# Optimization experiments

Measured on AMD Instinct MI355X. Metric: run time of the kernel, lower is better.

## Reference

```python
import jax, jax.numpy as jnp
import numpy as np

N_NODES = 100000
N_EDGES = 1600000
N_PAIRS = 1000000
IN_CH = 32
HID = 32


def glorot(key, shape):
    lim = float(np.sqrt(6.0 / (shape[0] + shape[1])))
    return jax.random.uniform(key, shape, jnp.float32, -lim, lim)


def setup_inputs() -> dict:
    key = jax.random.key(0)
    ks = jax.random.split(key, 9)
    x = jax.random.normal(ks[0], (N_NODES, IN_CH), jnp.float32)
    edge_index = jax.random.randint(ks[1], (2, N_EDGES), 0, N_NODES, jnp.int64)
    edge_pairs = jax.random.randint(ks[2], (N_PAIRS, 2), 0, N_NODES, jnp.int64)
    # SAGEConv params: lin_l acts on aggregated neighbors (has bias), lin_r on root.
    Wl1 = glorot(ks[3], (IN_CH, HID)); Wr1 = glorot(ks[4], (IN_CH, HID)); b1 = jnp.zeros((HID,), jnp.float32)
    Wl2 = glorot(ks[5], (HID, HID)); Wr2 = glorot(ks[6], (HID, HID)); b2 = jnp.zeros((HID,), jnp.float32)
    return {"x": x, "edge_index": edge_index, "edge_pairs": edge_pairs,
            "Wl1": Wl1, "Wr1": Wr1, "b1": b1, "Wl2": Wl2, "Wr2": Wr2, "b2": b2}


def sage_conv(x, src, dst, Wl, Wr, b):
    # mean-aggregate messages x[src] at dst, then linear + root linear
    msgs = x[src]                                             # [E, d] gather
    agg = jax.ops.segment_sum(msgs, dst, num_segments=N_NODES)  # [N, d]
    cnt = jax.ops.segment_sum(jnp.ones((src.shape[0],), x.dtype), dst, num_segments=N_NODES)
    agg = agg / jnp.maximum(cnt, 1.0)[:, None]
    return agg @ Wl + b + x @ Wr


def reference(x, edge_index, edge_pairs, Wl1, Wr1, b1, Wl2, Wr2, b2):
    src, dst = edge_index[0], edge_index[1]
    h = jax.nn.relu(sage_conv(x, src, dst, Wl1, Wr1, b1))  # dropout is identity in eval
    z = sage_conv(h, src, dst, Wl2, Wr2, b2)               # [N, HID]
    logits = jnp.sum(z[edge_pairs[:, 0]] * z[edge_pairs[:, 1]], axis=-1)  # [num_pairs]
    return logits
```

## Files before the change

### kernel.cpp

```cpp
#include <hip/hip_runtime.h>

typedef unsigned short ushort_t;

#define N_NODES 100000
#define N_EDGES 1600000
#define N_PAIRS 1000000
#define SCAN_CHUNK 1024
#define NB_SCAN ((N_NODES + SCAN_CHUNK - 1) / SCAN_CHUNK)
#define BSHIFT 9
#define BUCKET (1 << BSHIFT)
#define NBUCKET ((N_NODES + BUCKET - 1) >> BSHIFT)
#define SC_T 512
#define SC_K 8
#define EPB (SC_T * SC_K)

__device__ __forceinline__ float bf2f(ushort_t u) {
    return __uint_as_float(((unsigned)u) << 16);
}
__device__ __forceinline__ ushort_t f2bf(float f) {
    unsigned u = __float_as_uint(f);
    return (ushort_t)((u + 0x7FFFu + ((u >> 16) & 1u)) >> 16);
}

__global__ void cvt_kernel(const float* __restrict__ in, ushort_t* __restrict__ out) {
    int i = blockIdx.x * blockDim.x + threadIdx.x;
    if (i < N_NODES * 8) {
        float4 v = ((const float4*)in)[i];
        ushort4 o;
        o.x = f2bf(v.x); o.y = f2bf(v.y); o.z = f2bf(v.z); o.w = f2bf(v.w);
        ((ushort4*)out)[i] = o;
    }
}

__global__ void degree_kernel(const int* __restrict__ dst, int* __restrict__ deg) {
    int e = blockIdx.x * blockDim.x + threadIdx.x;
    if (e < N_EDGES) atomicAdd(&deg[dst[e]], 1);
}

__global__ void scan1_kernel(const int* __restrict__ deg,
                             int* __restrict__ incl,
                             int* __restrict__ bsum) {
    __shared__ int part[256];
    int t = threadIdx.x;
    int idx = blockIdx.x * SCAN_CHUNK + t * 4;
    int4 v = make_int4(0, 0, 0, 0);
    if (idx + 3 < N_NODES) {
        v = *(const int4*)(deg + idx);
    } else {
        if (idx + 0 < N_NODES) v.x = deg[idx + 0];
        if (idx + 1 < N_NODES) v.y = deg[idx + 1];
        if (idx + 2 < N_NODES) v.z = deg[idx + 2];
        if (idx + 3 < N_NODES) v.w = deg[idx + 3];
    }
    int s0 = v.x, s1 = s0 + v.y, s2 = s1 + v.z, s3 = s2 + v.w;
    part[t] = s3;
    __syncthreads();
    for (int off = 1; off < 256; off <<= 1) {
        int val = (t >= off) ? part[t - off] : 0;
        __syncthreads();
        part[t] += val;
        __syncthreads();
    }
    int excl = (t > 0) ? part[t - 1] : 0;
    if (idx + 0 < N_NODES) incl[idx + 0] = excl + s0;
    if (idx + 1 < N_NODES) incl[idx + 1] = excl + s1;
    if (idx + 2 < N_NODES) incl[idx + 2] = excl + s2;
    if (idx + 3 < N_NODES) incl[idx + 3] = excl + s3;
    if (t == 255) bsum[blockIdx.x] = part[255];
}

__global__ void scan2_kernel(int* __restrict__ bsum, int* __restrict__ offsets) {
    if (threadIdx.x == 0 && blockIdx.x == 0) {
        int run = 0;
        for (int i = 0; i < NB_SCAN; i++) {
            int t = bsum[i];
            bsum[i] = run;
            run += t;
        }
        offsets[N_NODES] = run;
    }
}

__global__ void scan3_kernel(const int* __restrict__ incl,
                             const int* __restrict__ deg,
                             const int* __restrict__ bsum,
                             int* __restrict__ offsets,
                             int* __restrict__ bcursor) {
    int i = blockIdx.x * blockDim.x + threadIdx.x;
    if (i < N_NODES) {
        int off = incl[i] - deg[i] + bsum[i / SCAN_CHUNK];
        offsets[i] = off;
        if ((i & (BUCKET - 1)) == 0) bcursor[i >> BSHIFT] = off;
    }
}

__global__ void bscatter_kernel(const int* __restrict__ src,
                                const int* __restrict__ dst,
                                int* __restrict__ bcursor,
                                int* __restrict__ bed) {
    __shared__ int hist[NBUCKET];
    __shared__ int base[NBUCKET];
    __shared__ int stage[EPB];
    __shared__ unsigned char sbkt[EPB];
    int t = threadIdx.x;
    long long e0 = (long long)blockIdx.x * EPB;
    int cnt = (int)((N_EDGES - e0 < EPB) ? (N_EDGES - e0) : EPB);

    for (int i = t; i < NBUCKET; i += SC_T) hist[i] = 0;
    __syncthreads();
    for (int i = t; i < cnt; i += SC_T) {
        int s = src[e0 + i];
        int d = dst[e0 + i];
        int b = d >> BSHIFT;
        stage[i] = (s << BSHIFT) | (d & (BUCKET - 1));
        sbkt[i] = (unsigned char)b;
        atomicAdd(&hist[b], 1);
    }
    __syncthreads();
    for (int i = t; i < NBUCKET; i += SC_T) {
        int c = hist[i];
        base[i] = c ? atomicAdd(&bcursor[i], c) : 0;
        hist[i] = 0;
    }
    __syncthreads();
    for (int i = t; i < cnt; i += SC_T) {
        int b = sbkt[i];
        int r = atomicAdd(&hist[b], 1);
        bed[base[b] + r] = stage[i];
    }
}

__global__ void ffill_kernel(const int* __restrict__ bed,
                             const int* __restrict__ offs,
                             int* __restrict__ csr) {
    __shared__ int cur[BUCKET];
    int b = blockIdx.x;
    int nbase = b << BSHIFT;
    int t = threadIdx.x;
    for (int i = t; i < BUCKET; i += blockDim.x) {
        int n = nbase + i;
        cur[i] = (n < N_NODES) ? offs[n] : 0;
    }
    __syncthreads();
    int nend = nbase + BUCKET;
    if (nend > N_NODES) nend = N_NODES;
    int beg = offs[nbase];
    int end = offs[nend];
    for (int i = beg + t; i < end; i += blockDim.x) {
        int p = bed[i];
        int pos = atomicAdd(&cur[p & (BUCKET - 1)], 1);
        csr[pos] = p >> BSHIFT;
    }
}

template <bool RELU, bool ROOT16>
__global__ void agg_linear_kernel(const ushort_t* __restrict__ feat16,
                                  const float* __restrict__ feat32,
                                  const int* __restrict__ csr,
                                  const int* __restrict__ offs,
                                  const float* __restrict__ Wl,
                                  const float* __restrict__ Wr,
                                  const float* __restrict__ b,
                                  ushort_t* __restrict__ out16) {
    __shared__ float sWl[1024], sWr[1024], sb[32];
    for (int i = threadIdx.x; i < 1024; i += blockDim.x) {
        sWl[i] = Wl[i];
        sWr[i] = Wr[i];
    }
    if (threadIdx.x < 32) sb[threadIdx.x] = b[threadIdx.x];
    __syncthreads();

    int g = threadIdx.x >> 5;
    int c = threadIdx.x & 31;
    int n = blockIdx.x * 8 + g;
    if (n >= N_NODES) return;

    const ushort_t* fc = feat16 + c;
    int beg = offs[n], end = offs[n + 1];
    float a0 = 0.f, a1 = 0.f, a2 = 0.f, a3 = 0.f;
    float a4 = 0.f, a5 = 0.f, a6 = 0.f, a7 = 0.f;
    int j = beg;
    for (; j + 7 < end; j += 8) {
        int s0 = csr[j + 0], s1 = csr[j + 1], s2 = csr[j + 2], s3 = csr[j + 3];
        int s4 = csr[j + 4], s5 = csr[j + 5], s6 = csr[j + 6], s7 = csr[j + 7];
        a0 += bf2f(fc[s0 * 32]); a1 += bf2f(fc[s1 * 32]);
        a2 += bf2f(fc[s2 * 32]); a3 += bf2f(fc[s3 * 32]);
        a4 += bf2f(fc[s4 * 32]); a5 += bf2f(fc[s5 * 32]);
        a6 += bf2f(fc[s6 * 32]); a7 += bf2f(fc[s7 * 32]);
    }
    for (; j < end; j++) a0 += bf2f(fc[csr[j] * 32]);
    float inv = 1.0f / (float)max(end - beg, 1);
    float acc = (((a0 + a1) + (a2 + a3)) + ((a4 + a5) + (a6 + a7))) * inv;
    float xr = ROOT16 ? bf2f(fc[n * 32]) : feat32[(long long)n * 32 + c];

    float o = sb[c];
#pragma unroll
    for (int i = 0; i < 32; i++) {
        float ai = __shfl(acc, i, 32);
        float xi = __shfl(xr, i, 32);
        o += ai * sWl[i * 32 + c] + xi * sWr[i * 32 + c];
    }
    float r = RELU ? fmaxf(o, 0.f) : o;
    out16[(long long)n * 32 + c] = f2bf(r);
}

__global__ void pair_kernel(const ushort_t* __restrict__ z16,
                            const int* __restrict__ pairs,
                            float* __restrict__ out) {
    int gid = blockIdx.x * blockDim.x + threadIdx.x;
    int q = gid >> 3;
    int l = gid & 7;
    if (q >= N_PAIRS / 4) return;
    const int4* pp = (const int4*)pairs;
    int4 i01 = pp[2 * q];
    int4 i23 = pp[2 * q + 1];
    const ushort_t* zl = z16 + l * 4;
    ushort4 a0 = *(const ushort4*)(zl + (long long)i01.x * 32);
    ushort4 b0 = *(const ushort4*)(zl + (long long)i01.y * 32);
    ushort4 a1 = *(const ushort4*)(zl + (long long)i01.z * 32);
    ushort4 b1 = *(const ushort4*)(zl + (long long)i01.w * 32);
    ushort4 a2 = *(const ushort4*)(zl + (long long)i23.x * 32);
    ushort4 b2 = *(const ushort4*)(zl + (long long)i23.y * 32);
    ushort4 a3 = *(const ushort4*)(zl + (long long)i23.z * 32);
    ushort4 b3 = *(const ushort4*)(zl + (long long)i23.w * 32);
    float d0 = bf2f(a0.x) * bf2f(b0.x) + bf2f(a0.y) * bf2f(b0.y)
             + bf2f(a0.z) * bf2f(b0.z) + bf2f(a0.w) * bf2f(b0.w);
    float d1 = bf2f(a1.x) * bf2f(b1.x) + bf2f(a1.y) * bf2f(b1.y)
             + bf2f(a1.z) * bf2f(b1.z) + bf2f(a1.w) * bf2f(b1.w);
    float d2 = bf2f(a2.x) * bf2f(b2.x) + bf2f(a2.y) * bf2f(b2.y)
             + bf2f(a2.z) * bf2f(b2.z) + bf2f(a2.w) * bf2f(b2.w);
    float d3 = bf2f(a3.x) * bf2f(b3.x) + bf2f(a3.y) * bf2f(b3.y)
             + bf2f(a3.z) * bf2f(b3.z) + bf2f(a3.w) * bf2f(b3.w);
#pragma unroll
    for (int off = 4; off >= 1; off >>= 1) {
        d0 += __shfl_xor(d0, off, 8);
        d1 += __shfl_xor(d1, off, 8);
        d2 += __shfl_xor(d2, off, 8);
        d3 += __shfl_xor(d3, off, 8);
    }
    if (l < 4) {
        float v = (l == 0) ? d0 : (l == 1) ? d1 : (l == 2) ? d2 : d3;
        out[4 * q + l] = v;
    }
}

extern "C" void kernel_launch(void* const* d_in, const int* in_sizes, int n_in,
                              void* d_out, int out_size, void* d_ws, size_t ws_size,
                              hipStream_t stream) {
    const float* x   = (const float*)d_in[0];
    const int*   ei  = (const int*)d_in[1];
    const int*   prs = (const int*)d_in[2];
    const float* Wl1 = (const float*)d_in[3];
    const float* Wr1 = (const float*)d_in[4];
    const float* b1  = (const float*)d_in[5];
    const float* Wl2 = (const float*)d_in[6];
    const float* Wr2 = (const float*)d_in[7];
    const float* b2  = (const float*)d_in[8];
    float* out = (float*)d_out;

    const int* src = ei;
    const int* dst = ei + N_EDGES;

    ushort_t* x16 = (ushort_t*)d_ws;
    ushort_t* h16 = x16 + (size_t)N_NODES * 32;
    ushort_t* z16 = h16 + (size_t)N_NODES * 32;
    int* csr     = (int*)(z16 + (size_t)N_NODES * 32);
    int* deg     = csr + N_EDGES;
    int* incl    = deg + N_NODES;
    int* offsets = incl + N_NODES;
    int* bsum    = offsets + (N_NODES + 1);
    int* bcursor = bsum + 128;
    int* bed     = (int*)z16;

    const int BT = 256;
    int cvt_blocks  = (N_NODES * 8 + BT - 1) / BT;
    int edge_blocks = (N_EDGES + BT - 1) / BT;
    int node_blocks = (N_NODES + BT - 1) / BT;
    int bsc_blocks  = (N_EDGES + EPB - 1) / EPB;
    int agg_blocks  = (N_NODES + 7) / 8;
    int pair_blocks = (int)(((long long)N_PAIRS * 2 + BT - 1) / BT);

    hipMemsetAsync(deg, 0, sizeof(int) * N_NODES, stream);
    cvt_kernel<<<cvt_blocks, BT, 0, stream>>>(x, x16);
    degree_kernel<<<edge_blocks, BT, 0, stream>>>(dst, deg);
    scan1_kernel<<<NB_SCAN, BT, 0, stream>>>(deg, incl, bsum);
    scan2_kernel<<<1, 64, 0, stream>>>(bsum, offsets);
    scan3_kernel<<<node_blocks, BT, 0, stream>>>(incl, deg, bsum, offsets, bcursor);
    bscatter_kernel<<<bsc_blocks, SC_T, 0, stream>>>(src, dst, bcursor, bed);
    ffill_kernel<<<NBUCKET, SC_T, 0, stream>>>(bed, offsets, csr);

    agg_linear_kernel<true, false><<<agg_blocks, BT, 0, stream>>>(
        x16, x, csr, offsets, Wl1, Wr1, b1, h16);
    agg_linear_kernel<false, true><<<agg_blocks, BT, 0, stream>>>(
        h16, nullptr, csr, offsets, Wl2, Wr2, b2, z16);

    pair_kernel<<<pair_blocks, BT, 0, stream>>>(z16, prs, out);
}
```

Measured before the change: 360.0 us.

## Split fused aggregate+linear into gather kernel and per-node-thread linear kernel

Splits the fused mean-aggregation and linear layer into two kernels. The gather kernel writes the bf16 mean aggregate to a new workspace buffer. A separate linear kernel then has each thread compute one node's full 32-wide output from registers with float4 weight reads from shared memory, which removes the per-output shuffles. This costs an extra round trip through global memory for the aggregate and two extra launches. The aggregate is also now rounded to bf16 before the matmul, and ffill's block size changes to 1024.

```diff
diff --git a/kernel.cpp b/kernel.cpp
--- a/kernel.cpp
+++ b/kernel.cpp
@@ -1,6 +1,7 @@
 #include <hip/hip_runtime.h>
 
 typedef unsigned short ushort_t;
+typedef unsigned int uint_t;
 
 #define N_NODES 100000
 #define N_EDGES 1600000
@@ -14,12 +15,26 @@
 #define SC_K 8
 #define EPB (SC_T * SC_K)
 
+#define COMP(v, k) ((k) == 0 ? (v).x : (k) == 1 ? (v).y : (k) == 2 ? (v).z : (v).w)
+
 __device__ __forceinline__ float bf2f(ushort_t u) {
     return __uint_as_float(((unsigned)u) << 16);
 }
 __device__ __forceinline__ ushort_t f2bf(float f) {
     unsigned u = __float_as_uint(f);
     return (ushort_t)((u + 0x7FFFu + ((u >> 16) & 1u)) >> 16);
+}
+__device__ __forceinline__ void load_bf16_row(const ushort_t* __restrict__ p, float* X) {
+    const uint4* rp = (const uint4*)p;
+#pragma unroll
+    for (int k = 0; k < 4; k++) {
+        uint4 r = rp[k];
+        uint_t u;
+        u = r.x; X[8 * k + 0] = __uint_as_float(u << 16); X[8 * k + 1] = __uint_as_float(u & 0xFFFF0000u);
+        u = r.y; X[8 * k + 2] = __uint_as_float(u << 16); X[8 * k + 3] = __uint_as_float(u & 0xFFFF0000u);
+        u = r.z; X[8 * k + 4] = __uint_as_float(u << 16); X[8 * k + 5] = __uint_as_float(u & 0xFFFF0000u);
+        u = r.w; X[8 * k + 6] = __uint_as_float(u << 16); X[8 * k + 7] = __uint_as_float(u & 0xFFFF0000u);
+    }
 }
 
 __global__ void cvt_kernel(const float* __restrict__ in, ushort_t* __restrict__ out) {
@@ -153,23 +168,10 @@
     }
 }
 
-template <bool RELU, bool ROOT16>
-__global__ void agg_linear_kernel(const ushort_t* __restrict__ feat16,
-                                  const float* __restrict__ feat32,
-                                  const int* __restrict__ csr,
-                                  const int* __restrict__ offs,
-                                  const float* __restrict__ Wl,
-                                  const float* __restrict__ Wr,
-                                  const float* __restrict__ b,
-                                  ushort_t* __restrict__ out16) {
-    __shared__ float sWl[1024], sWr[1024], sb[32];
-    for (int i = threadIdx.x; i < 1024; i += blockDim.x) {
-        sWl[i] = Wl[i];
-        sWr[i] = Wr[i];
-    }
-    if (threadIdx.x < 32) sb[threadIdx.x] = b[threadIdx.x];
-    __syncthreads();
-
+__global__ void gather_kernel(const ushort_t* __restrict__ feat16,
+                              const int* __restrict__ csr,
+                              const int* __restrict__ offs,
+                              ushort_t* __restrict__ agg16) {
     int g = threadIdx.x >> 5;
     int c = threadIdx.x & 31;
     int n = blockIdx.x * 8 + g;
@@ -191,17 +193,81 @@
     for (; j < end; j++) a0 += bf2f(fc[csr[j] * 32]);
     float inv = 1.0f / (float)max(end - beg, 1);
     float acc = (((a0 + a1) + (a2 + a3)) + ((a4 + a5) + (a6 + a7))) * inv;
-    float xr = ROOT16 ? bf2f(fc[n * 32]) : feat32[(long long)n * 32 + c];
-
-    float o = sb[c];
+    agg16[(long long)n * 32 + c] = f2bf(acc);
+}
+
+template <bool RELU, bool ROOT16>
+__global__ void linear_kernel(const ushort_t* __restrict__ agg16,
+                              const ushort_t* __restrict__ root16,
+                              const float* __restrict__ root32,
+                              const float* __restrict__ Wl,
+                              const float* __restrict__ Wr,
+                              const float* __restrict__ b,
+                              ushort_t* __restrict__ out16) {
+    __shared__ float4 sWl[256], sWr[256], sbv[8];
+    int t = threadIdx.x;
+    if (t < 256) {
+        sWl[t] = ((const float4*)Wl)[t];
+        sWr[t] = ((const float4*)Wr)[t];
+    }
+    if (t < 8) sbv[t] = ((const float4*)b)[t];
+    __syncthreads();
+
+    int n = blockIdx.x * blockDim.x + t;
+    if (n >= N_NODES) return;
+
+    float A[32];
+    load_bf16_row(agg16 + (long long)n * 32, A);
+
+    float X[32];
+    if (ROOT16) {
+        load_bf16_row(root16 + (long long)n * 32, X);
+    } else {
+        const float4* rp = (const float4*)(root32 + (long long)n * 32);
+#pragma unroll
+        for (int q = 0; q < 8; q++) {
+            float4 v = rp[q];
+            X[4 * q + 0] = v.x; X[4 * q + 1] = v.y; X[4 * q + 2] = v.z; X[4 * q + 3] = v.w;
+        }
+    }
+
+    float4 O[8];
+#pragma unroll
+    for (int q = 0; q < 8; q++) O[q] = sbv[q];
+
 #pragma unroll
     for (int i = 0; i < 32; i++) {
-        float ai = __shfl(acc, i, 32);
-        float xi = __shfl(xr, i, 32);
-        o += ai * sWl[i * 32 + c] + xi * sWr[i * 32 + c];
-    }
-    float r = RELU ? fmaxf(o, 0.f) : o;
-    out16[(long long)n * 32 + c] = f2bf(r);
+        float ai = A[i];
+        float xi = X[i];
+        const float4* wl = &sWl[i * 8];
+        const float4* wr = &sWr[i * 8];
+#pragma unroll
+        for (int q = 0; q < 8; q++) {
+            float4 wlv = wl[q];
+            float4 wrv = wr[q];
+            O[q].x += ai * wlv.x + xi * wrv.x;
+            O[q].y += ai * wlv.y + xi * wrv.y;
+            O[q].z += ai * wlv.z + xi * wrv.z;
+            O[q].w += ai * wlv.w + xi * wrv.w;
+        }
+    }
+
+    uint_t pk[16];
+#pragma unroll
+    for (int q = 0; q < 8; q++) {
+        float4 v = O[q];
+        if (RELU) {
+            v.x = fmaxf(v.x, 0.f); v.y = fmaxf(v.y, 0.f);
+            v.z = fmaxf(v.z, 0.f); v.w = fmaxf(v.w, 0.f);
+        }
+        pk[2 * q + 0] = (uint_t)f2bf(v.x) | ((uint_t)f2bf(v.y) << 16);
+        pk[2 * q + 1] = (uint_t)f2bf(v.z) | ((uint_t)f2bf(v.w) << 16);
+    }
+    uint4* op = (uint4*)(out16 + (long long)n * 32);
+    op[0] = make_uint4(pk[0], pk[1], pk[2], pk[3]);
+    op[1] = make_uint4(pk[4], pk[5], pk[6], pk[7]);
+    op[2] = make_uint4(pk[8], pk[9], pk[10], pk[11]);
+    op[3] = make_uint4(pk[12], pk[13], pk[14], pk[15]);
 }
 
 __global__ void pair_kernel(const ushort_t* __restrict__ z16,
@@ -261,23 +327,25 @@
     const int* src = ei;
     const int* dst = ei + N_EDGES;
 
-    ushort_t* x16 = (ushort_t*)d_ws;
-    ushort_t* h16 = x16 + (size_t)N_NODES * 32;
-    ushort_t* z16 = h16 + (size_t)N_NODES * 32;
-    int* csr     = (int*)(z16 + (size_t)N_NODES * 32);
-    int* deg     = csr + N_EDGES;
-    int* incl    = deg + N_NODES;
-    int* offsets = incl + N_NODES;
-    int* bsum    = offsets + (N_NODES + 1);
-    int* bcursor = bsum + 128;
-    int* bed     = (int*)z16;
+    ushort_t* x16   = (ushort_t*)d_ws;
+    ushort_t* h16   = x16 + (size_t)N_NODES * 32;
+    ushort_t* z16   = h16 + (size_t)N_NODES * 32;
+    int* csr        = (int*)(z16 + (size_t)N_NODES * 32);
+    ushort_t* agg16 = (ushort_t*)(csr + N_EDGES);
+    int* deg        = (int*)(agg16 + (size_t)N_NODES * 32);
+    int* incl       = deg + N_NODES;
+    int* offsets    = incl + N_NODES;
+    int* bsum       = offsets + (N_NODES + 1);
+    int* bcursor    = bsum + 128;
+    int* bed        = (int*)z16;
 
     const int BT = 256;
     int cvt_blocks  = (N_NODES * 8 + BT - 1) / BT;
     int edge_blocks = (N_EDGES + BT - 1) / BT;
     int node_blocks = (N_NODES + BT - 1) / BT;
     int bsc_blocks  = (N_EDGES + EPB - 1) / EPB;
-    int agg_blocks  = (N_NODES + 7) / 8;
+    int gat_blocks  = (N_NODES + 7) / 8;
+    int lin_blocks  = (N_NODES + BT - 1) / BT;
     int pair_blocks = (int)(((long long)N_PAIRS * 2 + BT - 1) / BT);
 
     hipMemsetAsync(deg, 0, sizeof(int) * N_NODES, stream);
@@ -287,12 +355,15 @@
     scan2_kernel<<<1, 64, 0, stream>>>(bsum, offsets);
     scan3_kernel<<<node_blocks, BT, 0, stream>>>(incl, deg, bsum, offsets, bcursor);
     bscatter_kernel<<<bsc_blocks, SC_T, 0, stream>>>(src, dst, bcursor, bed);
-    ffill_kernel<<<NBUCKET, SC_T, 0, stream>>>(bed, offsets, csr);
-
-    agg_linear_kernel<true, false><<<agg_blocks, BT, 0, stream>>>(
-        x16, x, csr, offsets, Wl1, Wr1, b1, h16);
-    agg_linear_kernel<false, true><<<agg_blocks, BT, 0, stream>>>(
-        h16, nullptr, csr, offsets, Wl2, Wr2, b2, z16);
+    ffill_kernel<<<NBUCKET, 1024, 0, stream>>>(bed, offsets, csr);
+
+    gather_kernel<<<gat_blocks, BT, 0, stream>>>(x16, csr, offsets, agg16);
+    linear_kernel<true, false><<<lin_blocks, BT, 0, stream>>>(
+        agg16, nullptr, x, Wl1, Wr1, b1, h16);
+
+    gather_kernel<<<gat_blocks, BT, 0, stream>>>(h16, csr, offsets, agg16);
+    linear_kernel<false, true><<<lin_blocks, BT, 0, stream>>>(
+        agg16, h16, nullptr, Wl2, Wr2, b2, z16);
 
     pair_kernel<<<pair_blocks, BT, 0, stream>>>(z16, prs, out);
 }
```

Measured after the change: 678.9 us. 88.6% more time.

## Replace per-node degree scan with bucket histogram and in-bucket offset scan

Applied to the files above, without the earlier changes.

Drops the per-node global degree atomics and the three-kernel scan over all nodes. Instead it builds a coarse bucket histogram in shared memory, scans the 196 bucket counts in a single block, and computes per-node CSR offsets inside ffill with a shared-memory count and scan per bucket. This cuts global atomics and launches, but ffill now runs 1024-thread blocks that read each bucket's edges twice.

```diff
diff --git a/kernel.cpp b/kernel.cpp
--- a/kernel.cpp
+++ b/kernel.cpp
@@ -1,12 +1,11 @@
 #include <hip/hip_runtime.h>
 
 typedef unsigned short ushort_t;
+typedef unsigned int uint_t;
 
 #define N_NODES 100000
 #define N_EDGES 1600000
 #define N_PAIRS 1000000
-#define SCAN_CHUNK 1024
-#define NB_SCAN ((N_NODES + SCAN_CHUNK - 1) / SCAN_CHUNK)
 #define BSHIFT 9
 #define BUCKET (1 << BSHIFT)
 #define NBUCKET ((N_NODES + BUCKET - 1) >> BSHIFT)
@@ -32,65 +31,38 @@
     }
 }
 
-__global__ void degree_kernel(const int* __restrict__ dst, int* __restrict__ deg) {
-    int e = blockIdx.x * blockDim.x + threadIdx.x;
-    if (e < N_EDGES) atomicAdd(&deg[dst[e]], 1);
-}
-
-__global__ void scan1_kernel(const int* __restrict__ deg,
-                             int* __restrict__ incl,
-                             int* __restrict__ bsum) {
-    __shared__ int part[256];
-    int t = threadIdx.x;
-    int idx = blockIdx.x * SCAN_CHUNK + t * 4;
-    int4 v = make_int4(0, 0, 0, 0);
-    if (idx + 3 < N_NODES) {
-        v = *(const int4*)(deg + idx);
-    } else {
-        if (idx + 0 < N_NODES) v.x = deg[idx + 0];
-        if (idx + 1 < N_NODES) v.y = deg[idx + 1];
-        if (idx + 2 < N_NODES) v.z = deg[idx + 2];
-        if (idx + 3 < N_NODES) v.w = deg[idx + 3];
-    }
-    int s0 = v.x, s1 = s0 + v.y, s2 = s1 + v.z, s3 = s2 + v.w;
-    part[t] = s3;
+__global__ void bhist_kernel(const int* __restrict__ dst, int* __restrict__ ghist) {
+    __shared__ int hist[NBUCKET];
+    int t = threadIdx.x;
+    for (int i = t; i < NBUCKET; i += blockDim.x) hist[i] = 0;
+    __syncthreads();
+    long long e0 = (long long)blockIdx.x * EPB;
+    long long e1 = e0 + EPB;
+    if (e1 > N_EDGES) e1 = N_EDGES;
+    for (long long i = e0 + t; i < e1; i += blockDim.x)
+        atomicAdd(&hist[dst[i] >> BSHIFT], 1);
+    __syncthreads();
+    for (int i = t; i < NBUCKET; i += blockDim.x)
+        if (hist[i]) atomicAdd(&ghist[i], hist[i]);
+}
+
+__global__ void bscan_kernel(const int* __restrict__ ghist, int* __restrict__ boff,
+                             int* __restrict__ bcursor, int* __restrict__ offsets) {
+    __shared__ int tmp[256];
+    int t = threadIdx.x;
+    tmp[t] = (t < NBUCKET) ? ghist[t] : 0;
     __syncthreads();
     for (int off = 1; off < 256; off <<= 1) {
-        int val = (t >= off) ? part[t - off] : 0;
-        __syncthreads();
-        part[t] += val;
-        __syncthreads();
-    }
-    int excl = (t > 0) ? part[t - 1] : 0;
-    if (idx + 0 < N_NODES) incl[idx + 0] = excl + s0;
-    if (idx + 1 < N_NODES) incl[idx + 1] = excl + s1;
-    if (idx + 2 < N_NODES) incl[idx + 2] = excl + s2;
-    if (idx + 3 < N_NODES) incl[idx + 3] = excl + s3;
-    if (t == 255) bsum[blockIdx.x] = part[255];
-}
-
-__global__ void scan2_kernel(int* __restrict__ bsum, int* __restrict__ offsets) {
-    if (threadIdx.x == 0 && blockIdx.x == 0) {
-        int run = 0;
-        for (int i = 0; i < NB_SCAN; i++) {
-            int t = bsum[i];
-            bsum[i] = run;
-            run += t;
-        }
-        offsets[N_NODES] = run;
-    }
-}
-
-__global__ void scan3_kernel(const int* __restrict__ incl,
-                             const int* __restrict__ deg,
-                             const int* __restrict__ bsum,
-                             int* __restrict__ offsets,
-                             int* __restrict__ bcursor) {
-    int i = blockIdx.x * blockDim.x + threadIdx.x;
-    if (i < N_NODES) {
-        int off = incl[i] - deg[i] + bsum[i / SCAN_CHUNK];
-        offsets[i] = off;
-        if ((i & (BUCKET - 1)) == 0) bcursor[i >> BSHIFT] = off;
+        int v = (t >= off) ? tmp[t - off] : 0;
+        __syncthreads();
+        tmp[t] += v;
+        __syncthreads();
+    }
+    int excl = (t > 0) ? tmp[t - 1] : 0;
+    if (t < NBUCKET) { boff[t] = excl; bcursor[t] = excl; }
+    if (t == NBUCKET) {
+        boff[t] = excl;
+        offsets[N_NODES] = excl;
     }
 }
 
@@ -131,22 +103,38 @@
 }
 
 __global__ void ffill_kernel(const int* __restrict__ bed,
-                             const int* __restrict__ offs,
+                             const int* __restrict__ boff,
+                             int* __restrict__ offsets,
                              int* __restrict__ csr) {
+    __shared__ int cnt[BUCKET];
+    __shared__ int scn[BUCKET];
     __shared__ int cur[BUCKET];
     int b = blockIdx.x;
-    int nbase = b << BSHIFT;
-    int t = threadIdx.x;
-    for (int i = t; i < BUCKET; i += blockDim.x) {
-        int n = nbase + i;
-        cur[i] = (n < N_NODES) ? offs[n] : 0;
-    }
-    __syncthreads();
-    int nend = nbase + BUCKET;
-    if (nend > N_NODES) nend = N_NODES;
-    int beg = offs[nbase];
-    int end = offs[nend];
-    for (int i = beg + t; i < end; i += blockDim.x) {
+    int t = threadIdx.x;
+    int base = boff[b], bend = boff[b + 1];
+
+    if (t < BUCKET) cnt[t] = 0;
+    __syncthreads();
+    for (int i = base + t; i < bend; i += blockDim.x)
+        atomicAdd(&cnt[bed[i] & (BUCKET - 1)], 1);
+    __syncthreads();
+    if (t < BUCKET) scn[t] = cnt[t];
+    __syncthreads();
+    for (int off = 1; off < BUCKET; off <<= 1) {
+        int v = 0;
+        if (t < BUCKET && t >= off) v = scn[t - off];
+        __syncthreads();
+        if (t < BUCKET) scn[t] += v;
+        __syncthreads();
+    }
+    if (t < BUCKET) {
+        int excl = scn[t] - cnt[t];
+        cur[t] = base + excl;
+        int n = (b << BSHIFT) + t;
+        if (n < N_NODES) offsets[n] = base + excl;
+    }
+    __syncthreads();
+    for (int i = base + t; i < bend; i += blockDim.x) {
         int p = bed[i];
         int pos = atomicAdd(&cur[p & (BUCKET - 1)], 1);
         csr[pos] = p >> BSHIFT;
@@ -264,30 +252,25 @@
     ushort_t* x16 = (ushort_t*)d_ws;
     ushort_t* h16 = x16 + (size_t)N_NODES * 32;
     ushort_t* z16 = h16 + (size_t)N_NODES * 32;
-    int* csr     = (int*)(z16 + (size_t)N_NODES * 32);
-    int* deg     = csr + N_EDGES;
-    int* incl    = deg + N_NODES;
-    int* offsets = incl + N_NODES;
-    int* bsum    = offsets + (N_NODES + 1);
-    int* bcursor = bsum + 128;
-    int* bed     = (int*)z16;
+    int* csr      = (int*)(z16 + (size_t)N_NODES * 32);
+    int* offsets  = csr + N_EDGES;
+    int* ghist    = offsets + (N_NODES + 1);
+    int* boff     = ghist + NBUCKET;
+    int* bcursor  = boff + (NBUCKET + 1);
+    int* bed      = (int*)z16;
 
     const int BT = 256;
     int cvt_blocks  = (N_NODES * 8 + BT - 1) / BT;
-    int edge_blocks = (N_EDGES + BT - 1) / BT;
-    int node_blocks = (N_NODES + BT - 1) / BT;
     int bsc_blocks  = (N_EDGES + EPB - 1) / EPB;
     int agg_blocks  = (N_NODES + 7) / 8;
     int pair_blocks = (int)(((long long)N_PAIRS * 2 + BT - 1) / BT);
 
-    hipMemsetAsync(deg, 0, sizeof(int) * N_NODES, stream);
+    hipMemsetAsync(ghist, 0, sizeof(int) * NBUCKET, stream);
     cvt_kernel<<<cvt_blocks, BT, 0, stream>>>(x, x16);
-    degree_kernel<<<edge_blocks, BT, 0, stream>>>(dst, deg);
-    scan1_kernel<<<NB_SCAN, BT, 0, stream>>>(deg, incl, bsum);
-    scan2_kernel<<<1, 64, 0, stream>>>(bsum, offsets);
-    scan3_kernel<<<node_blocks, BT, 0, stream>>>(incl, deg, bsum, offsets, bcursor);
+    bhist_kernel<<<bsc_blocks, BT, 0, stream>>>(dst, ghist);
+    bscan_kernel<<<1, 256, 0, stream>>>(ghist, boff, bcursor, offsets);
     bscatter_kernel<<<bsc_blocks, SC_T, 0, stream>>>(src, dst, bcursor, bed);
-    ffill_kernel<<<NBUCKET, SC_T, 0, stream>>>(bed, offsets, csr);
+    ffill_kernel<<<NBUCKET, 1024, 0, stream>>>(bed, boff, offsets, csr);
 
     agg_linear_kernel<true, false><<<agg_blocks, BT, 0, stream>>>(
         x16, x, csr, offsets, Wl1, Wr1, b1, h16);
```

Result: faster. 309.7 us (-14.0%).
